# Performance work log

Measured on AMD Instinct MI355X. Metric: run time of the kernel, lower is better.

Reference implementation:

```python
import jax, jax.numpy as jnp
import numpy as np

BN_EPS = 1e-5

def _maxpool2x2(t):
    # t: [B, C, H, W] -> [B, C, H//2, W//2]
    B, C, H, W = t.shape
    return t.reshape(B, C, H // 2, 2, W // 2, 2).max(axis=(3, 5))

def setup_inputs() -> dict:
    key = jax.random.key(0)
    ks = jax.random.split(key, 7)
    B, C, D, H, W = 16, 256, 128, 64, 64
    return {
        "x": jax.random.normal(ks[0], (B, C, H, W), dtype=jnp.float32),
        "g_w": jax.random.normal(ks[1], (D, C), dtype=jnp.float32) * (1.0 / np.sqrt(C)),
        "g_b": jax.random.normal(ks[2], (D,), dtype=jnp.float32) * 0.01,
        "w_w": jax.random.normal(ks[3], (C, D), dtype=jnp.float32) * (1.0 / np.sqrt(D)),
        "w_b": jax.random.normal(ks[4], (C,), dtype=jnp.float32) * 0.01,
        "gamma": jax.random.normal(ks[5], (C,), dtype=jnp.float32),
        "beta": jax.random.normal(ks[6], (C,), dtype=jnp.float32),
    }

def reference(x, g_w, g_b, w_w, w_b, gamma, beta):
    B, C, H, W = x.shape
    D = g_w.shape[0]
    # g branch: 1x1 conv C->D then 2x2 maxpool, flatten -> [B, M, D]
    g_x = jnp.einsum('bchw,dc->bdhw', x, g_w) + g_b[None, :, None, None]
    g_x = _maxpool2x2(g_x).reshape(B, D, -1).transpose(0, 2, 1)      # [B, M, D]
    # theta: raw x flattened -> [B, N, C]; phi: maxpooled x -> [B, C, M]
    theta = x.reshape(B, C, -1).transpose(0, 2, 1)                    # [B, N, C]
    phi = _maxpool2x2(x).reshape(B, C, -1)                            # [B, C, M]
    f = jnp.einsum('bnc,bcm->bnm', theta, phi)                        # [B, N, M]
    attn = jax.nn.softmax(f, axis=-1)
    y = jnp.einsum('bnm,bmd->bnd', attn, g_x)                         # [B, N, D]
    y = y.transpose(0, 2, 1).reshape(B, D, H, W)
    # W: 1x1 conv D->C then BatchNorm2d (training mode: batch stats)
    w_y = jnp.einsum('bdhw,cd->bchw', y, w_w) + w_b[None, :, None, None]
    mean = w_y.mean(axis=(0, 2, 3))
    var = w_y.var(axis=(0, 2, 3))  # biased, matching torch BN normalization
    w_y = (w_y - mean[None, :, None, None]) * jax.lax.rsqrt(var + BN_EPS)[None, :, None, None]
    w_y = w_y * gamma[None, :, None, None] + beta[None, :, None, None]
    return w_y + x
```

## Files before the change

kernel.cpp:

```cpp
#include <hip/hip_runtime.h>
#include <hip/hip_bf16.h>

typedef _Float16 half8 __attribute__((ext_vector_type(8)));
typedef float f32x4 __attribute__((ext_vector_type(4)));
typedef float f32x16 __attribute__((ext_vector_type(16)));
typedef unsigned uint4e __attribute__((ext_vector_type(4)));
typedef unsigned uint2e __attribute__((ext_vector_type(2)));

#define B_ 16
#define C_ 256
#define D_ 128
#define H_ 64
#define W_ 64
#define N_ 4096
#define M_ 1024
#define NCH 32

static constexpr size_t WS_PHI   = 0;
static constexpr size_t WS_GPOOL = WS_PHI   + (size_t)B_*M_*C_*2;
static constexpr size_t WS_Y     = WS_GPOOL + (size_t)B_*D_*M_*2;
static constexpr size_t WS_BNSUM = WS_Y     + (size_t)B_*N_*D_*2;
static constexpr size_t WS_BNSSQ = WS_BNSUM + (size_t)C_*4;
static constexpr size_t WS_PSUM  = WS_BNSSQ + (size_t)C_*4;
static constexpr size_t WS_PSSQ  = WS_PSUM  + (size_t)1024*256*4;
static constexpr size_t WS_GW16  = WS_PSSQ  + (size_t)1024*256*4;
static constexpr size_t WS_WW16  = WS_GW16  + (size_t)D_*C_*2;

typedef __attribute__((address_space(3))) void lds_vt;
typedef const __attribute__((address_space(1))) void gbl_vt;

__device__ __forceinline__ void gl2lds16(const void* g, void* s) {
  __builtin_amdgcn_global_load_lds((gbl_vt*)g, (lds_vt*)s, 16, 0, 0);
}

__device__ __forceinline__ unsigned pkrtz(float a, float b) {
  auto v = __builtin_amdgcn_cvt_pkrtz(a, b);
  return __builtin_bit_cast(unsigned, v);
}

__device__ __forceinline__ unsigned xor32_swap(unsigned v) {
#if __has_builtin(__builtin_amdgcn_permlane32_swap)
  auto pr = __builtin_amdgcn_permlane32_swap(v, v, false, false);
  uint2e p = __builtin_bit_cast(uint2e, pr);
  return (threadIdx.x & 32) ? p[0] : p[1];
#else
  return __shfl_xor(v, 32, 64);
#endif
}
__device__ __forceinline__ float xor32f(float v) {
  return __builtin_bit_cast(float, xor32_swap(__builtin_bit_cast(unsigned, v)));
}

__global__ __launch_bounds__(256) void conv16_kernel(
    const float* __restrict__ gw, const float* __restrict__ ww,
    _Float16* __restrict__ gw16, _Float16* __restrict__ ww16) {
  const int i = blockIdx.x*256 + threadIdx.x;
  gw16[i] = (_Float16)gw[i];
  ww16[i] = (_Float16)ww[i];
}

__global__ __launch_bounds__(512, 4) void fused_pre_kernel(
    const float* __restrict__ x, const _Float16* __restrict__ gw16,
    const float* __restrict__ g_b, _Float16* __restrict__ phi,
    _Float16* __restrict__ gpool) {
  const int i = blockIdx.x;
  const int b = blockIdx.y;
  const int t = threadIdx.x;
  const int w = t >> 6, l = t & 63, gq = (l >> 4) & 3, c16 = l & 15;
  const int wn = w & 3, wd = w >> 2;

  __shared__ _Float16 x_s[256][130];

  {
    const float* xb = x + (size_t)b*C_*N_ + (size_t)i*128;
#pragma unroll
    for (int it = 0; it < 16; ++it) {
      const int id = it*512 + t;
      const int c = id >> 5, nq = id & 31;
      float4 u = *(const float4*)(xb + (size_t)c*N_ + nq*4);
      unsigned* dst = (unsigned*)&x_s[c][nq*4];
      dst[0] = pkrtz(u.x, u.y);
      dst[1] = pkrtz(u.z, u.w);
    }
  }
  __syncthreads();

  f32x4 acc[4][2];
#pragma unroll
  for (int ds = 0; ds < 4; ++ds) {
    acc[ds][0] = (f32x4){0.f,0.f,0.f,0.f};
    acc[ds][1] = (f32x4){0.f,0.f,0.f,0.f};
  }

  const int nn0 = wn*16 + c16;
  const int mrow = i*32 + wn*8 + (c16 >> 1);

  for (int kk = 0; kk < 8; ++kk) {
    const int c0 = kk*32 + gq*8;
    half8 bf0, bf1;
#pragma unroll
    for (int j = 0; j < 8; ++j) {
      bf0[j] = x_s[c0 + j][nn0];
      bf1[j] = x_s[c0 + j][nn0 + 64];
    }
    if (wd == 0) {
      half8 pk_;
#pragma unroll
      for (int j = 0; j < 8; ++j) {
        float v = fmaxf((float)bf0[j], (float)bf1[j]);
        v = fmaxf(v, __shfl_xor(v, 1, 64));
        pk_[j] = (_Float16)v;
      }
      if (!(l & 1))
        *(half8*)(phi + ((size_t)b*M_ + mrow)*C_ + c0) = pk_;
    }
#pragma unroll
    for (int ds = 0; ds < 4; ++ds) {
      half8 af = *(const half8*)(gw16 + (size_t)((wd*4 + ds)*16 + c16)*C_ + c0);
      acc[ds][0] = __builtin_amdgcn_mfma_f32_16x16x32_f16(af, bf0, acc[ds][0], 0, 0, 0);
      acc[ds][1] = __builtin_amdgcn_mfma_f32_16x16x32_f16(af, bf1, acc[ds][1], 0, 0, 0);
    }
  }

#pragma unroll
  for (int ds = 0; ds < 4; ++ds) {
#pragma unroll
    for (int r = 0; r < 4; ++r) {
      const int d = (wd*4 + ds)*16 + gq*4 + r;
      float v = fmaxf(acc[ds][0][r], acc[ds][1][r]);
      v = fmaxf(v, __shfl_xor(v, 1, 64));
      if (!(l & 1))
        gpool[((size_t)b*D_ + d)*M_ + mrow] = (_Float16)(v + g_b[d]);
    }
  }
}

__global__ __launch_bounds__(512, 2) void attn_kernel(
    const float* __restrict__ x, const _Float16* __restrict__ phi,
    const _Float16* __restrict__ gpool, _Float16* __restrict__ y) {
  const int nt = blockIdx.x;
  const int b  = blockIdx.y;
  const int t  = threadIdx.x;
  const int w = t >> 6, l = t & 63, l31 = l & 31, lhi = l >> 5;
  const int nq = nt*256 + w*32 + l31;

  __shared__ alignas(16) _Float16 phi_s[3][32*256];
  __shared__ alignas(16) _Float16 gp_s[3][128*32];

  half8 qf[16];
#pragma unroll
  for (int kk = 0; kk < 16; ++kk) {
    const int cb = kk*16 + lhi*8;
    half8 q;
#pragma unroll
    for (int j = 0; j < 8; ++j) q[j] = (_Float16)x[((size_t)b*C_ + cb + j)*N_ + nq];
    qf[kk] = q;
  }

  f32x16 yacc0 = 0.f, yacc1 = 0.f, yacc2 = 0.f, yacc3 = 0.f;
  float m_run = -INFINITY, l_run = 0.f;

  auto stage = [&](int buf, int ch2) {
    const int m0 = ch2 * 32;
#pragma unroll
    for (int jj = 0; jj < 2; ++jj) {
      const int j = w*2 + jj;
      const char* src = (const char*)phi + ((size_t)(b*M_ + m0 + l31))*512 + (2*j + lhi)*16;
      gl2lds16(src, (char*)&phi_s[buf][0] + j*1024);
    }
    {
      const char* src = (const char*)gpool + (((size_t)(b*D_ + (w&1)*64 + l))*M_ + m0)*2 + (w>>1)*16;
      gl2lds16(src, (char*)&gp_s[buf][0] + w*1024);
    }
  };

  stage(0, 0);
  stage(1, 1);

  const char* pAbase = (const char*)&phi_s[0][0] + lhi*512 + l31*16;
  const char* pBbase = (const char*)&gp_s[0][0] + lhi*2048 + l31*16;

  for (int ch = 0; ch < NCH; ++ch) {
    const int cur = ch % 3;
    if (ch < NCH - 1) {
      asm volatile("s_waitcnt vmcnt(3)" ::: "memory");
    } else {
      asm volatile("s_waitcnt vmcnt(0)" ::: "memory");
    }
    __builtin_amdgcn_s_barrier();
    asm volatile("" ::: "memory");

    f32x16 fS = 0.f;
    const char* pA = pAbase + cur*16384;
    __builtin_amdgcn_s_setprio(1);
#pragma unroll
    for (int kk = 0; kk < 16; ++kk) {
      half8 a0 = *(const half8*)(pA + kk*1024);
      fS = __builtin_amdgcn_mfma_f32_32x32x16_f16(a0, qf[kk], fS, 0, 0, 0);
    }
    __builtin_amdgcn_s_setprio(0);

    float cmax = fS[0];
#pragma unroll
    for (int i = 1; i < 16; ++i) cmax = fmaxf(cmax, fS[i]);
    cmax = fmaxf(cmax, xor32f(cmax));
    if (__any(cmax - m_run > 8.0f)) {
      const float mn = fmaxf(m_run, cmax);
      const float sc = __expf(m_run - mn);
      m_run = mn;
      l_run *= sc;
      const int sci = __float_as_int(sc);
#pragma unroll
      for (int i = 0; i < 16; ++i) {
        const int qrow = (i & 3) + 8*(i >> 2) + 4*lhi;
        const float scn = __int_as_float(__builtin_amdgcn_ds_bpermute(4*qrow, sci));
        yacc0[i] *= scn; yacc1[i] *= scn; yacc2[i] *= scn; yacc3[i] *= scn;
      }
    }
    float p[16];
    float rs = 0.f;
#pragma unroll
    for (int i = 0; i < 16; ++i) { p[i] = __expf(fS[i] - m_run); rs += p[i]; }
    rs += xor32f(rs);
    l_run += rs;

    unsigned w0 = pkrtz(p[0],  p[1]),  w1 = pkrtz(p[2],  p[3]);
    unsigned w2 = pkrtz(p[4],  p[5]),  w3 = pkrtz(p[6],  p[7]);
    unsigned w4 = pkrtz(p[8],  p[9]),  w5 = pkrtz(p[10], p[11]);
    unsigned w6 = pkrtz(p[12], p[13]), w7 = pkrtz(p[14], p[15]);
    unsigned X0 = xor32_swap(w0), X1 = xor32_swap(w1);
    unsigned X2 = xor32_swap(w2), X3 = xor32_swap(w3);
    unsigned X4 = xor32_swap(w4), X5 = xor32_swap(w5);
    unsigned X6 = xor32_swap(w6), X7 = xor32_swap(w7);
    uint4e ua, ub;
    if (lhi == 0) {
      ua[0]=w0; ua[1]=w1; ua[2]=X0; ua[3]=X1;
      ub[0]=w4; ub[1]=w5; ub[2]=X4; ub[3]=X5;
    } else {
      ua[0]=X2; ua[1]=X3; ua[2]=w2; ua[3]=w3;
      ub[0]=X6; ub[1]=X7; ub[2]=w6; ub[3]=w7;
    }
    half8 pa0 = __builtin_bit_cast(half8, ua);
    half8 pa1 = __builtin_bit_cast(half8, ub);

    const char* pB = pBbase + cur*8192;
    __builtin_amdgcn_s_setprio(1);
#pragma unroll
    for (int dt = 0; dt < 4; ++dt) {
      half8 bv0 = *(const half8*)(pB + dt*512);
      half8 bv1 = *(const half8*)(pB + 4096 + dt*512);
      f32x16 acc = dt==0 ? yacc0 : dt==1 ? yacc1 : dt==2 ? yacc2 : yacc3;
      acc = __builtin_amdgcn_mfma_f32_32x32x16_f16(pa0, bv0, acc, 0, 0, 0);
      acc = __builtin_amdgcn_mfma_f32_32x32x16_f16(pa1, bv1, acc, 0, 0, 0);
      if (dt==0) yacc0 = acc; else if (dt==1) yacc1 = acc;
      else if (dt==2) yacc2 = acc; else yacc3 = acc;
    }
    __builtin_amdgcn_s_setprio(0);

    if (ch + 2 < NCH) stage((ch + 2) % 3, ch + 2);
  }

  {
    const float inv = 1.0f / l_run;
    const int invi = __float_as_int(inv);
#pragma unroll
    for (int i = 0; i < 16; ++i) {
      const int qrow = (i & 3) + 8*(i >> 2) + 4*lhi;
      const float invq = __int_as_float(__builtin_amdgcn_ds_bpermute(4*qrow, invi));
      const int n = nt*256 + w*32 + qrow;
      _Float16* yr = y + ((size_t)b*N_ + n)*D_ + l31;
      yr[0]  = (_Float16)(yacc0[i] * invq);
      yr[32] = (_Float16)(yacc1[i] * invq);
      yr[64] = (_Float16)(yacc2[i] * invq);
      yr[96] = (_Float16)(yacc3[i] * invq);
    }
  }
}

__global__ __launch_bounds__(256) void stats_partial_kernel(
    const _Float16* __restrict__ y, const _Float16* __restrict__ ww16,
    const float* __restrict__ w_b, float* __restrict__ psum,
    float* __restrict__ pssq) {
  const int nt = blockIdx.x, b = blockIdx.y, t = threadIdx.x;
  const int w = t >> 6, l = t & 63, g = l >> 4, c16 = l & 15;
  const int n0 = nt*64;

  f32x4 acc[4][4];
#pragma unroll
  for (int a = 0; a < 4; ++a)
#pragma unroll
    for (int n = 0; n < 4; ++n) acc[a][n] = (f32x4){0.f,0.f,0.f,0.f};

#pragma unroll
  for (int kk = 0; kk < 4; ++kk) {
    const int d0 = kk*32 + g*8;
    half8 af[4];
#pragma unroll
    for (int cs = 0; cs < 4; ++cs)
      af[cs] = *(const half8*)(ww16 + (size_t)(w*64 + cs*16 + c16)*D_ + d0);
#pragma unroll
    for (int ns = 0; ns < 4; ++ns) {
      const int nn = n0 + ns*16 + c16;
      half8 bf = *(const half8*)&y[((size_t)b*N_ + nn)*D_ + d0];
#pragma unroll
      for (int cs = 0; cs < 4; ++cs)
        acc[cs][ns] = __builtin_amdgcn_mfma_f32_16x16x32_f16(af[cs], bf, acc[cs][ns], 0, 0, 0);
    }
  }

  const int blk = b*64 + nt;
#pragma unroll
  for (int cs = 0; cs < 4; ++cs)
#pragma unroll
    for (int r = 0; r < 4; ++r) {
      const int c = w*64 + cs*16 + g*4 + r;
      const float wb = w_b[c];
      float s = 0.f, q = 0.f;
#pragma unroll
      for (int ns = 0; ns < 4; ++ns) {
        const float v = acc[cs][ns][r] + wb;
        s += v; q += v*v;
      }
      s += __shfl_xor(s, 1, 64); s += __shfl_xor(s, 2, 64);
      s += __shfl_xor(s, 4, 64); s += __shfl_xor(s, 8, 64);
      q += __shfl_xor(q, 1, 64); q += __shfl_xor(q, 2, 64);
      q += __shfl_xor(q, 4, 64); q += __shfl_xor(q, 8, 64);
      if (c16 == 0) {
        psum[blk*C_ + c] = s;
        pssq[blk*C_ + c] = q;
      }
    }
}

__global__ __launch_bounds__(256) void stats_reduce_kernel(
    const float* __restrict__ psum, const float* __restrict__ pssq,
    float* __restrict__ bnsum, float* __restrict__ bnssq) {
  const int t = threadIdx.x;
  const int ci = t & 31, bi = t >> 5;
  const int c = blockIdx.x*32 + ci;
  float s = 0.f, q = 0.f;
  for (int k = 0; k < 128; ++k) {
    const int row = bi + k*8;
    s += psum[row*C_ + c];
    q += pssq[row*C_ + c];
  }
  __shared__ float rs[8][32], rq[8][32];
  rs[bi][ci] = s; rq[bi][ci] = q;
  __syncthreads();
  if (bi == 0) {
    float S = 0.f, Q = 0.f;
#pragma unroll
    for (int k2 = 0; k2 < 8; ++k2) { S += rs[k2][ci]; Q += rq[k2][ci]; }
    bnsum[c] = S; bnssq[c] = Q;
  }
}

__global__ __launch_bounds__(256) void wconv_bn_kernel(
    const _Float16* __restrict__ y, const _Float16* __restrict__ ww16,
    const float* __restrict__ w_b, const float* __restrict__ bnsum,
    const float* __restrict__ bnssq, const float* __restrict__ gamma,
    const float* __restrict__ beta, const float* __restrict__ x,
    float* __restrict__ out) {
  const int nt = blockIdx.x, b = blockIdx.y, t = threadIdx.x;
  const int w = t >> 6, l = t & 63, g = l >> 4, c16 = l & 15;
  const int n0 = nt*64;

  f32x4 acc[4][4];
#pragma unroll
  for (int a = 0; a < 4; ++a)
#pragma unroll
    for (int n = 0; n < 4; ++n) acc[a][n] = (f32x4){0.f,0.f,0.f,0.f};

#pragma unroll
  for (int kk = 0; kk < 4; ++kk) {
    const int d0 = kk*32 + g*8;
    half8 af[4];
#pragma unroll
    for (int cs = 0; cs < 4; ++cs)
      af[cs] = *(const half8*)(ww16 + (size_t)(w*64 + cs*16 + c16)*D_ + d0);
#pragma unroll
    for (int ns = 0; ns < 4; ++ns) {
      const int nn = n0 + ns*16 + c16;
      half8 bf = *(const half8*)&y[((size_t)b*N_ + nn)*D_ + d0];
#pragma unroll
      for (int cs = 0; cs < 4; ++cs)
        acc[cs][ns] = __builtin_amdgcn_mfma_f32_16x16x32_f16(af[cs], bf, acc[cs][ns], 0, 0, 0);
    }
  }

  const float inv_cnt = 1.0f / (float)((size_t)B_ * N_);
#pragma unroll
  for (int cs = 0; cs < 4; ++cs) {
#pragma unroll
    for (int r = 0; r < 4; ++r) {
      const int c = w*64 + cs*16 + g*4 + r;
      const float wb  = w_b[c];
      const float mean = bnsum[c] * inv_cnt;
      const float var  = bnssq[c] * inv_cnt - mean*mean;
      const float istd = rsqrtf(var + 1e-5f);
      const float ga = gamma[c], be = beta[c];
#pragma unroll
      for (int ns = 0; ns < 4; ++ns) {
        const int n = n0 + ns*16 + c16;
        const size_t idx = ((size_t)b*C_ + c)*N_ + n;
        const float v = acc[cs][ns][r] + wb;
        out[idx] = (v - mean)*istd*ga + be + x[idx];
      }
    }
  }
}

extern "C" void kernel_launch(void* const* d_in, const int* in_sizes, int n_in,
                              void* d_out, int out_size, void* d_ws, size_t ws_size,
                              hipStream_t stream) {
  const float* x     = (const float*)d_in[0];
  const float* g_w   = (const float*)d_in[1];
  const float* g_b   = (const float*)d_in[2];
  const float* w_w   = (const float*)d_in[3];
  const float* w_b   = (const float*)d_in[4];
  const float* gamma = (const float*)d_in[5];
  const float* beta  = (const float*)d_in[6];
  float* out = (float*)d_out;

  char* ws = (char*)d_ws;
  _Float16* phi   = (_Float16*)(ws + WS_PHI);
  _Float16* gpool = (_Float16*)(ws + WS_GPOOL);
  _Float16* yb    = (_Float16*)(ws + WS_Y);
  float*    bnsum = (float*)(ws + WS_BNSUM);
  float*    bnssq = (float*)(ws + WS_BNSSQ);
  float*    psum  = (float*)(ws + WS_PSUM);
  float*    pssq  = (float*)(ws + WS_PSSQ);
  _Float16* gw16  = (_Float16*)(ws + WS_GW16);
  _Float16* ww16  = (_Float16*)(ws + WS_WW16);

  conv16_kernel<<<128, 256, 0, stream>>>(g_w, w_w, gw16, ww16);
  fused_pre_kernel<<<dim3(32, 16), 512, 0, stream>>>(x, gw16, g_b, phi, gpool);
  attn_kernel<<<dim3(16, 16), 512, 0, stream>>>(x, phi, gpool, yb);
  stats_partial_kernel<<<dim3(64, 16), 256, 0, stream>>>(yb, ww16, w_b, psum, pssq);
  stats_reduce_kernel<<<8, 256, 0, stream>>>(psum, pssq, bnsum, bnssq);
  wconv_bn_kernel<<<dim3(64, 16), 256, 0, stream>>>(yb, ww16, w_b, bnsum, bnssq, gamma, beta, x, out);
}
```

Before: 187.8 us.

## Split attention key dimension across two wave groups with flash-style merge

The attention kernel grows from 512 to 1024 threads per block. Two groups of 8 waves each process half of the key chunks (16 chunks each) with their own triple-buffered LDS region, then merge partial softmax statistics and accumulators through shared memory before writing y. The grid stays at 256 blocks, so this is meant to double the waves in flight per CU and hide latency in the serial chunk loop. The cost is a larger LDS footprint (144KB per block), an extra merge step through LDS, and duplicated query register loads in both groups. With 1024 threads the register budget per thread is tighter, which risks spilling.

```diff
diff --git a/kernel.cpp b/kernel.cpp
--- a/kernel.cpp
+++ b/kernel.cpp
@@ -14,7 +14,6 @@
 #define W_ 64
 #define N_ 4096
 #define M_ 1024
-#define NCH 32
 
 static constexpr size_t WS_PHI   = 0;
 static constexpr size_t WS_GPOOL = WS_PHI   + (size_t)B_*M_*C_*2;
@@ -135,17 +134,18 @@
   }
 }
 
-__global__ __launch_bounds__(512, 2) void attn_kernel(
+__global__ __launch_bounds__(1024, 4) void attn_kernel(
     const float* __restrict__ x, const _Float16* __restrict__ phi,
     const _Float16* __restrict__ gpool, _Float16* __restrict__ y) {
   const int nt = blockIdx.x;
   const int b  = blockIdx.y;
   const int t  = threadIdx.x;
-  const int w = t >> 6, l = t & 63, l31 = l & 31, lhi = l >> 5;
-  const int nq = nt*256 + w*32 + l31;
-
-  __shared__ alignas(16) _Float16 phi_s[3][32*256];
-  __shared__ alignas(16) _Float16 gp_s[3][128*32];
+  const int w = t >> 6, grp = w >> 3, wg = w & 7;
+  const int l = t & 63, l31 = l & 31, lhi = l >> 5;
+  const int nq = nt*256 + wg*32 + l31;
+
+  __shared__ alignas(16) char smem[147456];
+  char* gbase = smem + grp*73728;
 
   half8 qf[16];
 #pragma unroll
@@ -164,25 +164,25 @@
     const int m0 = ch2 * 32;
 #pragma unroll
     for (int jj = 0; jj < 2; ++jj) {
-      const int j = w*2 + jj;
+      const int j = wg*2 + jj;
       const char* src = (const char*)phi + ((size_t)(b*M_ + m0 + l31))*512 + (2*j + lhi)*16;
-      gl2lds16(src, (char*)&phi_s[buf][0] + j*1024);
+      gl2lds16(src, gbase + buf*16384 + j*1024);
     }
     {
-      const char* src = (const char*)gpool + (((size_t)(b*D_ + (w&1)*64 + l))*M_ + m0)*2 + (w>>1)*16;
-      gl2lds16(src, (char*)&gp_s[buf][0] + w*1024);
+      const char* src = (const char*)gpool + (((size_t)(b*D_ + (wg&1)*64 + l))*M_ + m0)*2 + (wg>>1)*16;
+      gl2lds16(src, gbase + 49152 + buf*8192 + wg*1024);
     }
   };
 
-  stage(0, 0);
-  stage(1, 1);
-
-  const char* pAbase = (const char*)&phi_s[0][0] + lhi*512 + l31*16;
-  const char* pBbase = (const char*)&gp_s[0][0] + lhi*2048 + l31*16;
-
-  for (int ch = 0; ch < NCH; ++ch) {
+  stage(0, grp*16);
+  stage(1, grp*16 + 1);
+
+  const char* pAbase = gbase + lhi*512 + l31*16;
+  const char* pBbase = gbase + 49152 + lhi*2048 + l31*16;
+
+  for (int ch = 0; ch < 16; ++ch) {
     const int cur = ch % 3;
-    if (ch < NCH - 1) {
+    if (ch < 15) {
       asm volatile("s_waitcnt vmcnt(3)" ::: "memory");
     } else {
       asm volatile("s_waitcnt vmcnt(0)" ::: "memory");
@@ -257,22 +257,45 @@
     }
     __builtin_amdgcn_s_setprio(0);
 
-    if (ch + 2 < NCH) stage((ch + 2) % 3, ch + 2);
-  }
-
-  {
-    const float inv = 1.0f / l_run;
+    if (ch + 2 < 16) stage((ch + 2) % 3, grp*16 + ch + 2);
+  }
+
+  __syncthreads();
+  float* mg = (float*)smem;
+  const int idx = wg*64 + l;
+  if (grp == 1) {
+#pragma unroll
+    for (int i = 0; i < 16; ++i) {
+      mg[(i)*512      + idx] = yacc0[i];
+      mg[(16 + i)*512 + idx] = yacc1[i];
+      mg[(32 + i)*512 + idx] = yacc2[i];
+      mg[(48 + i)*512 + idx] = yacc3[i];
+    }
+    mg[64*512 + idx] = m_run;
+    mg[65*512 + idx] = l_run;
+  }
+  __syncthreads();
+  if (grp == 0) {
+    const float mB = mg[64*512 + idx];
+    const float lB = mg[65*512 + idx];
+    const float mS = fmaxf(m_run, mB);
+    const float fa = __expf(m_run - mS);
+    const float fb = __expf(mB - mS);
+    const float inv = 1.0f / (l_run*fa + lB*fb);
+    const int fai = __float_as_int(fa), fbi = __float_as_int(fb);
     const int invi = __float_as_int(inv);
 #pragma unroll
     for (int i = 0; i < 16; ++i) {
       const int qrow = (i & 3) + 8*(i >> 2) + 4*lhi;
+      const float faq  = __int_as_float(__builtin_amdgcn_ds_bpermute(4*qrow, fai));
+      const float fbq  = __int_as_float(__builtin_amdgcn_ds_bpermute(4*qrow, fbi));
       const float invq = __int_as_float(__builtin_amdgcn_ds_bpermute(4*qrow, invi));
-      const int n = nt*256 + w*32 + qrow;
+      const int n = nt*256 + wg*32 + qrow;
       _Float16* yr = y + ((size_t)b*N_ + n)*D_ + l31;
-      yr[0]  = (_Float16)(yacc0[i] * invq);
-      yr[32] = (_Float16)(yacc1[i] * invq);
-      yr[64] = (_Float16)(yacc2[i] * invq);
-      yr[96] = (_Float16)(yacc3[i] * invq);
+      yr[0]  = (_Float16)((yacc0[i]*faq + mg[(i)*512      + idx]*fbq) * invq);
+      yr[32] = (_Float16)((yacc1[i]*faq + mg[(16 + i)*512 + idx]*fbq) * invq);
+      yr[64] = (_Float16)((yacc2[i]*faq + mg[(32 + i)*512 + idx]*fbq) * invq);
+      yr[96] = (_Float16)((yacc3[i]*faq + mg[(48 + i)*512 + idx]*fbq) * invq);
     }
   }
 }
@@ -435,7 +458,7 @@
 
   conv16_kernel<<<128, 256, 0, stream>>>(g_w, w_w, gw16, ww16);
   fused_pre_kernel<<<dim3(32, 16), 512, 0, stream>>>(x, gw16, g_b, phi, gpool);
-  attn_kernel<<<dim3(16, 16), 512, 0, stream>>>(x, phi, gpool, yb);
+  attn_kernel<<<dim3(16, 16), 1024, 0, stream>>>(x, phi, gpool, yb);
   stats_partial_kernel<<<dim3(64, 16), 256, 0, stream>>>(yb, ww16, w_b, psum, pssq);
   stats_reduce_kernel<<<8, 256, 0, stream>>>(psum, pssq, bnsum, bnssq);
   wconv_bn_kernel<<<dim3(64, 16), 256, 0, stream>>>(yb, ww16, w_b, bnsum, bnssq, gamma, beta, x, out);
```

Result: slower. 323.5 us (+72.3%).

## Split attention over key dimension into two halves and merge with log-sum-exp

Applied to the files above, without the earlier changes.

Splits the attention kernel's key (M) loop into two halves across a new grid z-dimension, so 512 blocks run instead of 256, which fills more CUs on the MI355X. Each half writes a normalized partial output plus its running max and sum, and a new merge kernel combines the two with softmax rescaling. The launch bounds hint is raised to 4 blocks per CU. This costs an extra pass over the y buffer, which is now twice as large, plus one more kernel launch. It also recomputes the query fragment loads in both halves.

```diff
diff --git a/kernel.cpp b/kernel.cpp
--- a/kernel.cpp
+++ b/kernel.cpp
@@ -14,12 +14,12 @@
 #define W_ 64
 #define N_ 4096
 #define M_ 1024
-#define NCH 32
 
 static constexpr size_t WS_PHI   = 0;
 static constexpr size_t WS_GPOOL = WS_PHI   + (size_t)B_*M_*C_*2;
 static constexpr size_t WS_Y     = WS_GPOOL + (size_t)B_*D_*M_*2;
-static constexpr size_t WS_BNSUM = WS_Y     + (size_t)B_*N_*D_*2;
+static constexpr size_t WS_ML    = WS_Y     + (size_t)2*B_*N_*D_*2;
+static constexpr size_t WS_BNSUM = WS_ML    + (size_t)2*B_*N_*8;
 static constexpr size_t WS_BNSSQ = WS_BNSUM + (size_t)C_*4;
 static constexpr size_t WS_PSUM  = WS_BNSSQ + (size_t)C_*4;
 static constexpr size_t WS_PSSQ  = WS_PSUM  + (size_t)1024*256*4;
@@ -135,11 +135,13 @@
   }
 }
 
-__global__ __launch_bounds__(512, 2) void attn_kernel(
+__global__ __launch_bounds__(512, 4) void attn_kernel(
     const float* __restrict__ x, const _Float16* __restrict__ phi,
-    const _Float16* __restrict__ gpool, _Float16* __restrict__ y) {
+    const _Float16* __restrict__ gpool, _Float16* __restrict__ ypart,
+    float2* __restrict__ mlbuf) {
   const int nt = blockIdx.x;
   const int b  = blockIdx.y;
+  const int hf = blockIdx.z;
   const int t  = threadIdx.x;
   const int w = t >> 6, l = t & 63, l31 = l & 31, lhi = l >> 5;
   const int nq = nt*256 + w*32 + l31;
@@ -174,15 +176,15 @@
     }
   };
 
-  stage(0, 0);
-  stage(1, 1);
+  stage(0, hf*16);
+  stage(1, hf*16 + 1);
 
   const char* pAbase = (const char*)&phi_s[0][0] + lhi*512 + l31*16;
   const char* pBbase = (const char*)&gp_s[0][0] + lhi*2048 + l31*16;
 
-  for (int ch = 0; ch < NCH; ++ch) {
+  for (int ch = 0; ch < 16; ++ch) {
     const int cur = ch % 3;
-    if (ch < NCH - 1) {
+    if (ch < 15) {
       asm volatile("s_waitcnt vmcnt(3)" ::: "memory");
     } else {
       asm volatile("s_waitcnt vmcnt(0)" ::: "memory");
@@ -257,24 +259,50 @@
     }
     __builtin_amdgcn_s_setprio(0);
 
-    if (ch + 2 < NCH) stage((ch + 2) % 3, ch + 2);
+    if (ch + 2 < 16) stage((ch + 2) % 3, hf*16 + ch + 2);
   }
 
   {
     const float inv = 1.0f / l_run;
     const int invi = __float_as_int(inv);
+    _Float16* yh = ypart + (size_t)hf*B_*N_*D_;
 #pragma unroll
     for (int i = 0; i < 16; ++i) {
       const int qrow = (i & 3) + 8*(i >> 2) + 4*lhi;
       const float invq = __int_as_float(__builtin_amdgcn_ds_bpermute(4*qrow, invi));
       const int n = nt*256 + w*32 + qrow;
-      _Float16* yr = y + ((size_t)b*N_ + n)*D_ + l31;
+      _Float16* yr = yh + ((size_t)b*N_ + n)*D_ + l31;
       yr[0]  = (_Float16)(yacc0[i] * invq);
       yr[32] = (_Float16)(yacc1[i] * invq);
       yr[64] = (_Float16)(yacc2[i] * invq);
       yr[96] = (_Float16)(yacc3[i] * invq);
     }
-  }
+    if (lhi == 0)
+      mlbuf[(size_t)hf*B_*N_ + (size_t)b*N_ + nq] = make_float2(m_run, l_run);
+  }
+}
+
+__global__ __launch_bounds__(256) void merge_kernel(
+    _Float16* __restrict__ ypart, const float2* __restrict__ mlbuf) {
+  const int t = threadIdx.x;
+  const size_t row = (size_t)blockIdx.x*16 + (t >> 4);
+  const int c16 = t & 15;
+  const float2 a = mlbuf[row];
+  const float2 bm = mlbuf[(size_t)B_*N_ + row];
+  const float ms = fmaxf(a.x, bm.x);
+  const float w0 = a.y * __expf(a.x - ms);
+  const float w1 = bm.y * __expf(bm.x - ms);
+  const float inv = 1.0f / (w0 + w1);
+  const float f0 = w0 * inv, f1 = w1 * inv;
+  _Float16* p0 = ypart + row*D_ + c16*8;
+  const _Float16* p1 = p0 + (size_t)B_*N_*D_;
+  half8 v0 = *(const half8*)p0;
+  half8 v1 = *(const half8*)p1;
+  half8 o;
+#pragma unroll
+  for (int j = 0; j < 8; ++j)
+    o[j] = (_Float16)((float)v0[j]*f0 + (float)v1[j]*f1);
+  *(half8*)p0 = o;
 }
 
 __global__ __launch_bounds__(256) void stats_partial_kernel(
@@ -426,6 +454,7 @@
   _Float16* phi   = (_Float16*)(ws + WS_PHI);
   _Float16* gpool = (_Float16*)(ws + WS_GPOOL);
   _Float16* yb    = (_Float16*)(ws + WS_Y);
+  float2*   mlb   = (float2*)(ws + WS_ML);
   float*    bnsum = (float*)(ws + WS_BNSUM);
   float*    bnssq = (float*)(ws + WS_BNSSQ);
   float*    psum  = (float*)(ws + WS_PSUM);
@@ -435,7 +464,8 @@
 
   conv16_kernel<<<128, 256, 0, stream>>>(g_w, w_w, gw16, ww16);
   fused_pre_kernel<<<dim3(32, 16), 512, 0, stream>>>(x, gw16, g_b, phi, gpool);
-  attn_kernel<<<dim3(16, 16), 512, 0, stream>>>(x, phi, gpool, yb);
+  attn_kernel<<<dim3(16, 16, 2), 512, 0, stream>>>(x, phi, gpool, yb, mlb);
+  merge_kernel<<<4096, 256, 0, stream>>>(yb, mlb);
   stats_partial_kernel<<<dim3(64, 16), 256, 0, stream>>>(yb, ww16, w_b, psum, pssq);
   stats_reduce_kernel<<<8, 256, 0, stream>>>(psum, pssq, bnsum, bnssq);
   wconv_bn_kernel<<<dim3(64, 16), 256, 0, stream>>>(yb, ww16, w_b, bnsum, bnssq, gamma, beta, x, out);
```

After: 323.9 us. +72.5%, slower.
